# Performance work log

Hardware: AMD Instinct MI355X
Metric: run time of the kernel (lower is better)

The kernel has to match this reference:

```python
import jax, jax.numpy as jnp
import numpy as np

N = 400000      # total atoms
MAXD = 4        # max degree
NDEG = MAXD + 1 # degrees 0..4 (DeepChem min_degree=0)
F0 = 75         # ConvMolFeaturizer atom feature size
B = 16384       # number of graphs (batch_size)
NT = 12         # n_tasks
DIMS = [F0, 15, 20, 27, 36]


def setup_inputs() -> dict:
    key = jax.random.key(0)
    ks = jax.random.split(key, 40)
    inp = {}
    inp["atom_features"] = jax.random.normal(ks[0], (N, F0), jnp.float32)
    i = 1
    for l in range(4):
        fi, fo = DIMS[l], DIMS[l + 1]
        inp[f"Ws{l+1}"] = jax.random.normal(ks[i], (NDEG, fi, fo), jnp.float32) * 0.1; i += 1
        inp[f"Wn{l+1}"] = jax.random.normal(ks[i], (NDEG, fi, fo), jnp.float32) * 0.1; i += 1
        inp[f"b{l+1}"] = jax.random.normal(ks[i], (NDEG, fo), jnp.float32) * 0.1; i += 1
    inp["Wd2"] = jax.random.normal(ks[i], (2 * DIMS[-1], NT * 2), jnp.float32) * 0.1; i += 1
    inp["bd2"] = jnp.zeros((NT * 2,), jnp.float32)
    inp["Wl1"] = jax.random.normal(ks[i], (2 * NT, 96), jnp.float32) * 0.1; i += 1
    inp["bl1"] = jnp.zeros((96,), jnp.float32)
    inp["g1"] = jnp.ones((96,), jnp.float32)
    inp["be1"] = jnp.zeros((96,), jnp.float32)
    inp["Wl2"] = jax.random.normal(ks[i], (96, 63), jnp.float32) * 0.1; i += 1
    inp["bl2"] = jnp.zeros((63,), jnp.float32)
    inp["g2"] = jnp.ones((63,), jnp.float32)
    inp["be2"] = jnp.zeros((63,), jnp.float32)
    inp["Wl3"] = jax.random.normal(ks[i], (63, 138), jnp.float32) * 0.1; i += 1
    inp["bl3"] = jnp.zeros((138,), jnp.float32)
    inp["neighbor_list"] = jax.random.randint(ks[i], (N, MAXD), 0, N, dtype=jnp.int32); i += 1
    inp["degree"] = jax.random.randint(ks[i], (N,), 0, NDEG, dtype=jnp.int32); i += 1
    inp["membership"] = jnp.sort(jax.random.randint(ks[i], (N,), 0, B, dtype=jnp.int32)); i += 1
    inp["batch_size"] = B
    return inp


def _graph_conv(x, Ws, Wn, b, nbr, deg_onehot, nmask):
    # gather neighbor features and sum over (masked) neighbor slots: [N, Fin]
    nsum = (x[nbr] * nmask).sum(axis=1)
    # per-degree affine (DeepChem: separate self/neighbor weights per degree)
    pre = (jnp.einsum('nf,dfg->ndg', x, Ws)
           + jnp.einsum('nf,dfg->ndg', nsum, Wn)
           + b[None])                              # [N, NDEG, Fout]
    out = jnp.einsum('nd,ndg->ng', deg_onehot, pre)  # select row for atom's degree
    return jax.nn.selu(out)


def _bn(x, g, b, eps=1e-5):
    m = x.mean(axis=0)
    v = x.var(axis=0)
    return (x - m) * jax.lax.rsqrt(v + eps) * g + b


def reference(atom_features, Ws1, Wn1, b1, Ws2, Wn2, b2, Ws3, Wn3, b3,
              Ws4, Wn4, b4, Wd2, bd2, Wl1, bl1, g1, be1,
              Wl2, bl2, g2, be2, Wl3, bl3,
              neighbor_list, degree, membership, batch_size):
    deg_onehot = jax.nn.one_hot(degree, NDEG, dtype=atom_features.dtype)
    nmask = (jnp.arange(MAXD, dtype=degree.dtype)[None, :] < degree[:, None])
    nmask = nmask.astype(atom_features.dtype)[:, :, None]          # [N, MAXD, 1]

    x = _graph_conv(atom_features, Ws1, Wn1, b1, neighbor_list, deg_onehot, nmask)
    x = _graph_conv(x, Ws2, Wn2, b2, neighbor_list, deg_onehot, nmask)
    x = _graph_conv(x, Ws3, Wn3, b3, neighbor_list, deg_onehot, nmask)
    x = _graph_conv(x, Ws4, Wn4, b4, neighbor_list, deg_onehot, nmask)

    # GraphGather readout: concat(segment_sum, segment_max) then selu
    s = jax.ops.segment_sum(x, membership, num_segments=batch_size,
                            indices_are_sorted=True)
    m = jax.ops.segment_max(x, membership, num_segments=batch_size,
                            indices_are_sorted=True)
    m = jnp.where(jnp.isfinite(m), m, 0.0)  # empty graphs -> 0
    r = jax.nn.selu(jnp.concatenate([s, m], axis=1))               # [B, 72]

    logits = (r @ Wd2 + bd2).reshape(batch_size, -1, 2)            # [B, NT, 2]
    p = jax.nn.softmax(logits, axis=-1).reshape(batch_size, -1)    # [B, 2*NT]

    h = jax.nn.relu(_bn(p @ Wl1 + bl1, g1, be1))
    h = jax.nn.relu(_bn(h @ Wl2 + bl2, g2, be2))
    return jax.nn.sigmoid(h @ Wl3 + bl3)                            # [B, 138]
```

## Files before the change

kernel.cpp:

```cpp
#include <hip/hip_runtime.h>
#include <hip/hip_bf16.h>

#define N_ATOMS 400000
#define MAX_D   4
#define NDEG_   5
#define B_GR    16384
#define NTASK   12
#define AT      256
#define TA      64
#define NTHR    512
#define PADCAP  401408

typedef float float4u __attribute__((ext_vector_type(4), aligned(4)));

__device__ __forceinline__ float selu_f(float x) {
    const float a = 1.6732632423543772f, s = 1.0507009873554805f;
    return x > 0.f ? s * x : s * a * (__expf(x) - 1.f);
}

__device__ __forceinline__ unsigned short f2bf(float x) {
    unsigned int u = __float_as_uint(x);
    return (unsigned short)((u + 0x7FFFu + ((u >> 16) & 1u)) >> 16);
}
__device__ __forceinline__ float bf2f(unsigned int s) {
    return __uint_as_float(s << 16);
}

__global__ void zero_kernel(int* ctr) {
    if (threadIdx.x < 10) ctr[threadIdx.x] = 0;
}

__launch_bounds__(256)
__global__ void fill_kernel(int* idx, int* degs_s, int4* nbrs_s, int4* nbro_s) {
    const int e = blockIdx.x * 256 + threadIdx.x;
    if (e < PADCAP) {
        idx[e] = -1;
        degs_s[e] = -1;
        nbrs_s[e] = make_int4(0, 0, 0, 0);
        nbro_s[e] = make_int4(0, 0, 0, 0);
    }
}

__launch_bounds__(256)
__global__ void hist_kernel(const int* __restrict__ deg, int* ctr) {
    __shared__ int h[NDEG_];
    if (threadIdx.x < NDEG_) h[threadIdx.x] = 0;
    __syncthreads();
    for (int i = blockIdx.x * 256 + threadIdx.x; i < N_ATOMS; i += gridDim.x * 256)
        atomicAdd(&h[deg[i]], 1);
    __syncthreads();
    if (threadIdx.x < NDEG_ && h[threadIdx.x]) atomicAdd(&ctr[threadIdx.x], h[threadIdx.x]);
}

__global__ void offsets_kernel(int* ctr) {
    if (threadIdx.x == 0) {
        int run = 0;
        for (int d = 0; d < NDEG_; ++d) {
            ctr[10 + d] = run;
            run += ctr[d];
            run = (run + AT - 1) & ~(AT - 1);
        }
        ctr[15] = run;
    }
}

__launch_bounds__(256)
__global__ void scatter_kernel(const int* __restrict__ deg, int* ctr,
                               int* idx, int* rank, int* degs_s) {
    __shared__ int h[NDEG_];
    __shared__ int base[NDEG_];
    const int i = blockIdx.x * 256 + threadIdx.x;
    const int d = (i < N_ATOMS) ? deg[i] : -1;
    if (threadIdx.x < NDEG_) h[threadIdx.x] = 0;
    __syncthreads();
    int intra = 0;
    if (i < N_ATOMS) intra = atomicAdd(&h[d], 1);
    __syncthreads();
    if (threadIdx.x < NDEG_ && h[threadIdx.x] > 0)
        base[threadIdx.x] = atomicAdd(&ctr[5 + threadIdx.x], h[threadIdx.x]);
    __syncthreads();
    if (i < N_ATOMS) {
        const int p = ctr[10 + d] + base[d] + intra;
        idx[p] = i;
        rank[i] = p;
        degs_s[p] = d;
    }
}

__launch_bounds__(256)
__global__ void nbrprep_kernel(const int* __restrict__ nbr, const int* __restrict__ rank,
                               int4* __restrict__ nbrs_s, int4* __restrict__ nbro_s) {
    const int i = blockIdx.x * 256 + threadIdx.x;
    if (i >= N_ATOMS) return;
    const int p = rank[i];
    const int4 nb = *reinterpret_cast<const int4*>(nbr + (size_t)i * MAX_D);
    nbro_s[p] = nb;
    nbrs_s[p] = make_int4(rank[nb.x], rank[nb.y], rank[nb.z], rank[nb.w]);
}

__launch_bounds__(NTHR)
__global__ void conv1_project(const float* __restrict__ af,
                              const float* __restrict__ Ws1,
                              const float* __restrict__ Wn1,
                              const float* __restrict__ b1,
                              const int*   __restrict__ degs_s,
                              const int*   __restrict__ idx,
                              float*       __restrict__ S,
                              unsigned short* __restrict__ Z)
{
    __shared__ float xt[TA][76];
    __shared__ int s_a[TA];

    const int pb = blockIdx.x * TA;
    const int dfirst = degs_s[pb];
    if (dfirst < 0) return;
    const int tid = threadIdx.x;

    if (tid < TA) {
        int a = idx[pb + tid];
        s_a[tid] = (a < 0) ? 0 : a;
    }
    __syncthreads();

    #pragma unroll 2
    for (int e = tid; e < TA * 18; e += NTHR) {
        const int al = e / 18, f4 = e - al * 18;
        *(float4u*)&xt[al][f4 * 4] = *(const float4u*)(af + (size_t)s_a[al] * 75 + f4 * 4);
    }
    for (int e = tid; e < TA * 3; e += NTHR) {
        const int al = e / 3, r = e - al * 3;
        xt[al][72 + r] = af[(size_t)s_a[al] * 75 + 72 + r];
    }
    __syncthreads();

    const int w = __builtin_amdgcn_readfirstlane(tid >> 6);
    const int l = tid & 63;

    if (w < 4) {
        const float* __restrict__ wn = Wn1 + (size_t)(w + 1) * 75 * 15;
        float acc[15];
        #pragma unroll
        for (int o = 0; o < 15; ++o) acc[o] = 0.f;
        for (int f4 = 0; f4 < 18; ++f4) {
            const float4u xv = *(const float4u*)&xt[l][f4 * 4];
            #pragma unroll
            for (int k = 0; k < 4; ++k) {
                const float* __restrict__ wf = wn + (f4 * 4 + k) * 15;
                #pragma unroll
                for (int o = 0; o < 15; ++o) acc[o] = fmaf(xv[k], wf[o], acc[o]);
            }
        }
        #pragma unroll
        for (int k = 0; k < 3; ++k) {
            const float xv = xt[l][72 + k];
            const float* __restrict__ wf = wn + (72 + k) * 15;
            #pragma unroll
            for (int o = 0; o < 15; ++o) acc[o] = fmaf(xv, wf[o], acc[o]);
        }
        unsigned short zr[16];
        #pragma unroll
        for (int o = 0; o < 15; ++o) zr[o] = f2bf(acc[o]);
        zr[15] = 0;
        unsigned short* zp = Z + ((size_t)w * PADCAP + pb + l) * 16;
        ((int4*)zp)[0] = ((const int4*)zr)[0];
        ((int4*)zp)[1] = ((const int4*)zr)[1];
    } else {
        const int o0 = (w - 4) * 4;
        const int d = __builtin_amdgcn_readfirstlane(dfirst);
        const float* __restrict__ wsp = Ws1 + (size_t)d * 75 * 15 + o0;
        const float* __restrict__ bb  = b1 + d * 15 + o0;
        float acc[4];
        #pragma unroll
        for (int oo = 0; oo < 4; ++oo) acc[oo] = (o0 + oo < 15) ? bb[oo] : 0.f;
        for (int f4 = 0; f4 < 18; ++f4) {
            const float4u xv = *(const float4u*)&xt[l][f4 * 4];
            #pragma unroll
            for (int k = 0; k < 4; ++k) {
                const float* __restrict__ wf = wsp + (f4 * 4 + k) * 15;
                #pragma unroll
                for (int oo = 0; oo < 4; ++oo)
                    if (o0 + oo < 15) acc[oo] = fmaf(xv[k], wf[oo], acc[oo]);
            }
        }
        #pragma unroll
        for (int k = 0; k < 3; ++k) {
            const float xv = xt[l][72 + k];
            const float* __restrict__ wf = wsp + (72 + k) * 15;
            #pragma unroll
            for (int oo = 0; oo < 4; ++oo)
                if (o0 + oo < 15) acc[oo] = fmaf(xv, wf[oo], acc[oo]);
        }
        float4u sv = {acc[0], acc[1], acc[2], acc[3]};
        *(float4u*)(S + (size_t)(pb + l) * 16 + o0) = sv;
    }
}

template<int DEG>
__device__ __forceinline__ void combine_body(const float* __restrict__ S,
                                             const unsigned short* __restrict__ Z,
                                             const int4* __restrict__ nbrs_s,
                                             float* __restrict__ x1, int p)
{
    float acc[16];
    #pragma unroll
    for (int q = 0; q < 4; ++q)
        *(float4u*)&acc[q * 4] = *(const float4u*)(S + (size_t)p * 16 + q * 4);

    if (DEG > 0) {
        const int4 nb = nbrs_s[p];
        const int nbid[4] = {nb.x, nb.y, nb.z, nb.w};
        #pragma unroll
        for (int j = 0; j < DEG; ++j) {
            const unsigned short* zp = Z + ((size_t)(DEG - 1) * PADCAP + nbid[j]) * 16;
            unsigned int zz[8];
            *(int4*)&zz[0] = ((const int4*)zp)[0];
            *(int4*)&zz[4] = ((const int4*)zp)[1];
            #pragma unroll
            for (int o = 0; o < 15; ++o)
                acc[o] += bf2f((zz[o >> 1] >> ((o & 1) * 16)) & 0xffffu);
        }
    }
    #pragma unroll
    for (int o = 0; o < 15; ++o)
        x1[(size_t)p * 15 + o] = selu_f(acc[o]);
}

__launch_bounds__(256)
__global__ void conv1_combine(const float* __restrict__ S,
                              const unsigned short* __restrict__ Z,
                              const int4* __restrict__ nbrs_s,
                              const int*  __restrict__ degs_s,
                              float*      __restrict__ x1)
{
    const int base = blockIdx.x * 256;
    const int dfirst = degs_s[base];
    if (dfirst < 0) return;
    const int p = base + threadIdx.x;
    switch (__builtin_amdgcn_readfirstlane(dfirst)) {
    case 0: combine_body<0>(S, Z, nbrs_s, x1, p); break;
    case 1: combine_body<1>(S, Z, nbrs_s, x1, p); break;
    case 2: combine_body<2>(S, Z, nbrs_s, x1, p); break;
    case 3: combine_body<3>(S, Z, nbrs_s, x1, p); break;
    default: combine_body<4>(S, Z, nbrs_s, x1, p); break;
    }
}

template<int FI, int FIP, int FO, bool SCATTER_OUT, int DEG>
__device__ __forceinline__ void conv_body(const float* __restrict__ x,
                                          const float* __restrict__ Ws,
                                          const float* __restrict__ Wn,
                                          const float* __restrict__ bias,
                                          const int*   __restrict__ idx,
                                          float*       __restrict__ outs,
                                          float (*__restrict__ xt)[FIP],
                                          float (*__restrict__ nt)[FIP],
                                          const int*  s_a,
                                          const int4* s_nb,
                                          int pb, int tid)
{
    #pragma unroll 2
    for (int e = tid; e < TA * FI; e += NTHR) {
        const int al = e / FI, f = e - al * FI;
        const int4 nb = s_nb[al];
        const float xv = x[(size_t)s_a[al] * FI + f];
        float s = 0.f;
        if (DEG > 0) s += x[(size_t)nb.x * FI + f];
        if (DEG > 1) s += x[(size_t)nb.y * FI + f];
        if (DEG > 2) s += x[(size_t)nb.z * FI + f];
        if (DEG > 3) s += x[(size_t)nb.w * FI + f];
        xt[al][f] = xv;
        nt[al][f] = s;
    }
    __syncthreads();

    const int w = __builtin_amdgcn_readfirstlane(tid >> 6);
    const int l = tid & 63;
    constexpr int OPG = (FO + 7) / 8;
    const int o0 = w * OPG;
    const float* __restrict__ wsd = Ws + (DEG * FI) * FO + o0;
    const float* __restrict__ wnd = Wn + (DEG * FI) * FO + o0;
    const float* __restrict__ bb  = bias + DEG * FO + o0;

    float acc[OPG];
    #pragma unroll
    for (int oo = 0; oo < OPG; ++oo)
        acc[oo] = (o0 + oo < FO) ? bb[oo] : 0.f;

    for (int f = 0; f < FI; ++f) {
        const float xv = xt[l][f];
        const float nv = nt[l][f];
        const float* __restrict__ wsf = wsd + f * FO;
        const float* __restrict__ wnf = wnd + f * FO;
        #pragma unroll
        for (int oo = 0; oo < OPG; ++oo) {
            if (o0 + oo < FO)
                acc[oo] = fmaf(xv, wsf[oo], fmaf(nv, wnf[oo], acc[oo]));
        }
    }

    int row; bool store;
    if (SCATTER_OUT) { row = idx[pb + l]; store = (row >= 0); }
    else             { row = pb + l;      store = true; }
    if (store) {
        float* __restrict__ orow = outs + (size_t)row * FO + o0;
        #pragma unroll
        for (int oo = 0; oo < OPG; ++oo)
            if (o0 + oo < FO) orow[oo] = selu_f(acc[oo]);
    }
}

template<int FI, int FIP, int FO, bool SCATTER_OUT>
__launch_bounds__(NTHR)
__global__ void conv_fused5(const float* __restrict__ x,
                            const int4*  __restrict__ nbr_,
                            const float* __restrict__ Ws,
                            const float* __restrict__ Wn,
                            const float* __restrict__ bias,
                            const int*   __restrict__ degs_s,
                            const int*   __restrict__ idx,
                            float*       __restrict__ outs)
{
    __shared__ float xt[TA][FIP];
    __shared__ float nt[TA][FIP];
    __shared__ int   s_a[TA];
    __shared__ int4  s_nb[TA];

    const int pb = blockIdx.x * TA;
    const int dfirst = degs_s[pb];
    if (dfirst < 0) return;
    const int tid = threadIdx.x;

    if (tid < TA) {
        const int p = pb + tid;
        s_a[tid] = p;
        s_nb[tid] = nbr_[p];
    }
    __syncthreads();

    switch (__builtin_amdgcn_readfirstlane(dfirst)) {
    case 0: conv_body<FI, FIP, FO, SCATTER_OUT, 0>(x, Ws, Wn, bias, idx, outs, xt, nt, s_a, s_nb, pb, tid); break;
    case 1: conv_body<FI, FIP, FO, SCATTER_OUT, 1>(x, Ws, Wn, bias, idx, outs, xt, nt, s_a, s_nb, pb, tid); break;
    case 2: conv_body<FI, FIP, FO, SCATTER_OUT, 2>(x, Ws, Wn, bias, idx, outs, xt, nt, s_a, s_nb, pb, tid); break;
    case 3: conv_body<FI, FIP, FO, SCATTER_OUT, 3>(x, Ws, Wn, bias, idx, outs, xt, nt, s_a, s_nb, pb, tid); break;
    default: conv_body<FI, FIP, FO, SCATTER_OUT, 4>(x, Ws, Wn, bias, idx, outs, xt, nt, s_a, s_nb, pb, tid); break;
    }
}

__launch_bounds__(64)
__global__ void readout_kernel(const float* __restrict__ x4o,
                               const int*   __restrict__ mem,
                               const float* __restrict__ Wd2,
                               const float* __restrict__ bd2,
                               float*       __restrict__ p)
{
    const int g = blockIdx.x;
    const int t = threadIdx.x;

    int lo = 0, hi = N_ATOMS;
    while (lo < hi) { int mid = (lo + hi) >> 1; if (mem[mid] < g) lo = mid + 1; else hi = mid; }
    int lo2 = lo, hi2 = N_ATOMS;
    while (lo2 < hi2) { int mid = (lo2 + hi2) >> 1; if (mem[mid] < g + 1) lo2 = mid + 1; else hi2 = mid; }

    __shared__ float r[72];
    if (t < 36) {
        float s = 0.f, m = -3.4e38f;
        for (int a = lo; a < lo2; ++a) {
            float v = x4o[(size_t)a * 36 + t];
            s += v;
            m = fmaxf(m, v);
        }
        if (lo2 == lo) m = 0.f;
        r[t]      = selu_f(s);
        r[36 + t] = selu_f(m);
    }
    __syncthreads();
    if (t < 24) {
        float acc = bd2[t];
        #pragma unroll
        for (int f = 0; f < 72; ++f) acc += r[f] * Wd2[f * 24 + t];
        float part = __shfl_xor(acc, 1);
        p[g * 24 + t] = 1.f / (1.f + __expf(part - acc));
    }
}

__launch_bounds__(256)
__global__ void dense1_kernel(const float* __restrict__ p,
                              const float* __restrict__ Wl1,
                              const float* __restrict__ bl1,
                              float*       __restrict__ y1)
{
    const int idx = blockIdx.x * 256 + threadIdx.x;
    if (idx >= B_GR * 96) return;
    const int row = idx / 96, c = idx - row * 96;
    float acc = bl1[c];
    const float* pr = p + row * 24;
    #pragma unroll
    for (int f = 0; f < 24; ++f) acc += pr[f] * Wl1[f * 96 + c];
    y1[idx] = acc;
}

template<int C>
__launch_bounds__(256)
__global__ void stats_kernel(const float* __restrict__ y, float* __restrict__ st)
{
    const int c = blockIdx.x;
    float s = 0.f, q = 0.f;
    for (int r = threadIdx.x; r < B_GR; r += 256) {
        const float v = y[r * C + c];
        s += v; q += v * v;
    }
    __shared__ float ss[256], qq[256];
    ss[threadIdx.x] = s; qq[threadIdx.x] = q;
    __syncthreads();
    for (int off = 128; off > 0; off >>= 1) {
        if (threadIdx.x < off) {
            ss[threadIdx.x] += ss[threadIdx.x + off];
            qq[threadIdx.x] += qq[threadIdx.x + off];
        }
        __syncthreads();
    }
    if (threadIdx.x == 0) {
        const float mean = ss[0] / (float)B_GR;
        const float var  = qq[0] / (float)B_GR - mean * mean;
        st[c]     = mean;
        st[C + c] = rsqrtf(var + 1e-5f);
    }
}

__launch_bounds__(256)
__global__ void dense2_kernel(const float* __restrict__ y1,
                              const float* __restrict__ st1,
                              const float* __restrict__ g1,
                              const float* __restrict__ be1,
                              const float* __restrict__ Wl2,
                              const float* __restrict__ bl2,
                              float*       __restrict__ y2)
{
    __shared__ float h[4 * 96];
    const int r0 = blockIdx.x * 4;
    for (int e = threadIdx.x; e < 4 * 96; e += 256) {
        const int rr = e / 96, c = e - rr * 96;
        float v = y1[(r0 + rr) * 96 + c];
        v = (v - st1[c]) * st1[96 + c] * g1[c] + be1[c];
        h[e] = fmaxf(v, 0.f);
    }
    __syncthreads();
    for (int e = threadIdx.x; e < 4 * 63; e += 256) {
        const int rr = e / 63, o = e - rr * 63;
        float acc = bl2[o];
        #pragma unroll
        for (int f = 0; f < 96; ++f) acc += h[rr * 96 + f] * Wl2[f * 63 + o];
        y2[(r0 + rr) * 63 + o] = acc;
    }
}

__launch_bounds__(320)
__global__ void dense3_kernel(const float* __restrict__ y2,
                              const float* __restrict__ st2,
                              const float* __restrict__ g2,
                              const float* __restrict__ be2,
                              const float* __restrict__ Wl3,
                              const float* __restrict__ bl3,
                              float*       __restrict__ out)
{
    __shared__ float h[2 * 63];
    const int r0 = blockIdx.x * 2;
    for (int e = threadIdx.x; e < 2 * 63; e += 320) {
        const int rr = e / 63, c = e - rr * 63;
        float v = y2[(r0 + rr) * 63 + c];
        v = (v - st2[c]) * st2[63 + c] * g2[c] + be2[c];
        h[e] = fmaxf(v, 0.f);
    }
    __syncthreads();
    for (int e = threadIdx.x; e < 2 * 138; e += 320) {
        const int rr = e / 138, o = e - rr * 138;
        float acc = bl3[o];
        #pragma unroll
        for (int f = 0; f < 63; ++f) acc += h[rr * 63 + f] * Wl3[f * 138 + o];
        out[(r0 + rr) * 138 + o] = 1.f / (1.f + __expf(-acc));
    }
}

extern "C" void kernel_launch(void* const* d_in, const int* in_sizes, int n_in,
                              void* d_out, int out_size, void* d_ws, size_t ws_size,
                              hipStream_t stream)
{
    (void)in_sizes; (void)n_in; (void)out_size; (void)ws_size;

    const float* af  = (const float*)d_in[0];
    const float* Ws1 = (const float*)d_in[1];
    const float* Wn1 = (const float*)d_in[2];
    const float* b1  = (const float*)d_in[3];
    const float* Ws2 = (const float*)d_in[4];
    const float* Wn2 = (const float*)d_in[5];
    const float* b2  = (const float*)d_in[6];
    const float* Ws3 = (const float*)d_in[7];
    const float* Wn3 = (const float*)d_in[8];
    const float* b3  = (const float*)d_in[9];
    const float* Ws4 = (const float*)d_in[10];
    const float* Wn4 = (const float*)d_in[11];
    const float* b4  = (const float*)d_in[12];
    const float* Wd2 = (const float*)d_in[13];
    const float* bd2 = (const float*)d_in[14];
    const float* Wl1 = (const float*)d_in[15];
    const float* bl1 = (const float*)d_in[16];
    const float* g1  = (const float*)d_in[17];
    const float* be1 = (const float*)d_in[18];
    const float* Wl2 = (const float*)d_in[19];
    const float* bl2 = (const float*)d_in[20];
    const float* g2  = (const float*)d_in[21];
    const float* be2 = (const float*)d_in[22];
    const float* Wl3 = (const float*)d_in[23];
    const float* bl3 = (const float*)d_in[24];
    const int*   nbr = (const int*)d_in[25];
    const int*   deg = (const int*)d_in[26];
    const int*   mem = (const int*)d_in[27];

    float* ws = (float*)d_ws;
    float* A = ws;
    float* B = A + (size_t)PADCAP * 27;
    float* Zr = B + (size_t)PADCAP * 36;
    int*   idx    = (int*)(Zr + (size_t)PADCAP * 32);
    int*   rank   = idx + PADCAP;
    int*   degs_s = rank + N_ATOMS;
    int4*  nbrs_s = (int4*)(degs_s + PADCAP);
    int4*  nbro_s = nbrs_s + PADCAP;
    int*   ctr    = (int*)(nbro_s + PADCAP);

    float* x1  = A;
    float* Sb  = B;
    unsigned short* Zb = (unsigned short*)Zr;
    float* x2  = B;
    float* x3  = A;
    float* x4o = B;
    float* p   = A;
    float* y1  = A + 393216;
    float* y2  = A + 393216 + 1572864;
    float* st1 = A + 393216 + 1572864 + 1032192;
    float* st2 = st1 + 192;

    zero_kernel<<<1, 16, 0, stream>>>(ctr);
    fill_kernel<<<PADCAP / 256, 256, 0, stream>>>(idx, degs_s, nbrs_s, nbro_s);
    hist_kernel<<<1024, 256, 0, stream>>>(deg, ctr);
    offsets_kernel<<<1, 1, 0, stream>>>(ctr);
    scatter_kernel<<<(N_ATOMS + 255) / 256, 256, 0, stream>>>(deg, ctr, idx, rank, degs_s);
    nbrprep_kernel<<<(N_ATOMS + 255) / 256, 256, 0, stream>>>(nbr, rank, nbrs_s, nbro_s);

    conv1_project<<<PADCAP / TA, NTHR, 0, stream>>>(af, Ws1, Wn1, b1, degs_s, idx, Sb, Zb);
    conv1_combine<<<PADCAP / 256, 256, 0, stream>>>(Sb, Zb, nbrs_s, degs_s, x1);

    conv_fused5<15, 17, 20, false><<<PADCAP / TA, NTHR, 0, stream>>>
        (x1, nbrs_s, Ws2, Wn2, b2, degs_s, idx, x2);
    conv_fused5<20, 21, 27, false><<<PADCAP / TA, NTHR, 0, stream>>>
        (x2, nbrs_s, Ws3, Wn3, b3, degs_s, idx, x3);
    conv_fused5<27, 29, 36, true ><<<PADCAP / TA, NTHR, 0, stream>>>
        (x3, nbrs_s, Ws4, Wn4, b4, degs_s, idx, x4o);

    readout_kernel<<<B_GR, 64, 0, stream>>>(x4o, mem, Wd2, bd2, p);

    dense1_kernel<<<(B_GR * 96) / 256, 256, 0, stream>>>(p, Wl1, bl1, y1);
    stats_kernel<96><<<96, 256, 0, stream>>>(y1, st1);
    dense2_kernel<<<B_GR / 4, 256, 0, stream>>>(y1, st1, g1, be1, Wl2, bl2, y2);
    stats_kernel<63><<<63, 256, 0, stream>>>(y2, st2);
    dense3_kernel<<<B_GR / 2, 320, 0, stream>>>(y2, st2, g2, be2, Wl3, bl3, (float*)d_out);
}
```

Baseline: 710.8 us.

## Merge conv1 projection waves and split combine across four threads per atom

The layer-1 projection kernel drops from 8 to 4 waves per block. Each wave now computes both its neighbor-weight Z projection and a 4-column slice of the self projection, so each LDS row of features is read once for both. The combine kernel assigns four threads per atom, each handling a 4-output slice with 8-byte gathers, which raises parallelism and shortens per-thread work. Per-thread register pressure in projection goes up and block count per atom tile is unchanged, so occupancy and latency hiding shift.

```diff
diff --git a/kernel.cpp b/kernel.cpp
--- a/kernel.cpp
+++ b/kernel.cpp
@@ -98,7 +98,7 @@
     nbrs_s[p] = make_int4(rank[nb.x], rank[nb.y], rank[nb.z], rank[nb.w]);
 }
 
-__launch_bounds__(NTHR)
+__launch_bounds__(256)
 __global__ void conv1_project(const float* __restrict__ af,
                               const float* __restrict__ Ws1,
                               const float* __restrict__ Wn1,
@@ -123,11 +123,11 @@
     __syncthreads();
 
     #pragma unroll 2
-    for (int e = tid; e < TA * 18; e += NTHR) {
+    for (int e = tid; e < TA * 18; e += 256) {
         const int al = e / 18, f4 = e - al * 18;
         *(float4u*)&xt[al][f4 * 4] = *(const float4u*)(af + (size_t)s_a[al] * 75 + f4 * 4);
     }
-    for (int e = tid; e < TA * 3; e += NTHR) {
+    for (int e = tid; e < TA * 3; e += 256) {
         const int al = e / 3, r = e - al * 3;
         xt[al][72 + r] = af[(size_t)s_a[al] * 75 + 72 + r];
     }
@@ -135,94 +135,90 @@
 
     const int w = __builtin_amdgcn_readfirstlane(tid >> 6);
     const int l = tid & 63;
-
-    if (w < 4) {
-        const float* __restrict__ wn = Wn1 + (size_t)(w + 1) * 75 * 15;
-        float acc[15];
-        #pragma unroll
-        for (int o = 0; o < 15; ++o) acc[o] = 0.f;
-        for (int f4 = 0; f4 < 18; ++f4) {
-            const float4u xv = *(const float4u*)&xt[l][f4 * 4];
+    const int d = __builtin_amdgcn_readfirstlane(dfirst);
+    const int o0 = w * 4;
+    const float* __restrict__ wn  = Wn1 + (size_t)(w + 1) * 75 * 15;
+    const float* __restrict__ wsp = Ws1 + (size_t)d * 75 * 15 + o0;
+    const float* __restrict__ bb  = b1 + d * 15 + o0;
+
+    float accz[15];
+    #pragma unroll
+    for (int o = 0; o < 15; ++o) accz[o] = 0.f;
+    float accs[4];
+    #pragma unroll
+    for (int oo = 0; oo < 4; ++oo) accs[oo] = (o0 + oo < 15) ? bb[oo] : 0.f;
+
+    #pragma unroll
+    for (int g = 0; g < 6; ++g) {
+        const float4u c0 = *(const float4u*)&xt[l][(g * 3 + 0) * 4];
+        const float4u c1 = *(const float4u*)&xt[l][(g * 3 + 1) * 4];
+        const float4u c2 = *(const float4u*)&xt[l][(g * 3 + 2) * 4];
+        #pragma unroll
+        for (int c = 0; c < 3; ++c) {
+            const float4u xv = (c == 0) ? c0 : (c == 1) ? c1 : c2;
             #pragma unroll
             for (int k = 0; k < 4; ++k) {
-                const float* __restrict__ wf = wn + (f4 * 4 + k) * 15;
+                const int f = (g * 3 + c) * 4 + k;
+                const float* __restrict__ wfz = wn + f * 15;
+                const float* __restrict__ wfs = wsp + f * 15;
                 #pragma unroll
-                for (int o = 0; o < 15; ++o) acc[o] = fmaf(xv[k], wf[o], acc[o]);
+                for (int o = 0; o < 15; ++o) accz[o] = fmaf(xv[k], wfz[o], accz[o]);
+                #pragma unroll
+                for (int oo = 0; oo < 4; ++oo)
+                    if (o0 + oo < 15) accs[oo] = fmaf(xv[k], wfs[oo], accs[oo]);
             }
         }
-        #pragma unroll
-        for (int k = 0; k < 3; ++k) {
-            const float xv = xt[l][72 + k];
-            const float* __restrict__ wf = wn + (72 + k) * 15;
-            #pragma unroll
-            for (int o = 0; o < 15; ++o) acc[o] = fmaf(xv, wf[o], acc[o]);
-        }
-        unsigned short zr[16];
-        #pragma unroll
-        for (int o = 0; o < 15; ++o) zr[o] = f2bf(acc[o]);
-        zr[15] = 0;
-        unsigned short* zp = Z + ((size_t)w * PADCAP + pb + l) * 16;
-        ((int4*)zp)[0] = ((const int4*)zr)[0];
-        ((int4*)zp)[1] = ((const int4*)zr)[1];
-    } else {
-        const int o0 = (w - 4) * 4;
-        const int d = __builtin_amdgcn_readfirstlane(dfirst);
-        const float* __restrict__ wsp = Ws1 + (size_t)d * 75 * 15 + o0;
-        const float* __restrict__ bb  = b1 + d * 15 + o0;
-        float acc[4];
-        #pragma unroll
-        for (int oo = 0; oo < 4; ++oo) acc[oo] = (o0 + oo < 15) ? bb[oo] : 0.f;
-        for (int f4 = 0; f4 < 18; ++f4) {
-            const float4u xv = *(const float4u*)&xt[l][f4 * 4];
-            #pragma unroll
-            for (int k = 0; k < 4; ++k) {
-                const float* __restrict__ wf = wsp + (f4 * 4 + k) * 15;
-                #pragma unroll
-                for (int oo = 0; oo < 4; ++oo)
-                    if (o0 + oo < 15) acc[oo] = fmaf(xv[k], wf[oo], acc[oo]);
-            }
-        }
-        #pragma unroll
-        for (int k = 0; k < 3; ++k) {
-            const float xv = xt[l][72 + k];
-            const float* __restrict__ wf = wsp + (72 + k) * 15;
-            #pragma unroll
-            for (int oo = 0; oo < 4; ++oo)
-                if (o0 + oo < 15) acc[oo] = fmaf(xv, wf[oo], acc[oo]);
-        }
-        float4u sv = {acc[0], acc[1], acc[2], acc[3]};
-        *(float4u*)(S + (size_t)(pb + l) * 16 + o0) = sv;
-    }
+    }
+    #pragma unroll
+    for (int k = 0; k < 3; ++k) {
+        const float xv = xt[l][72 + k];
+        const float* __restrict__ wfz = wn + (72 + k) * 15;
+        const float* __restrict__ wfs = wsp + (72 + k) * 15;
+        #pragma unroll
+        for (int o = 0; o < 15; ++o) accz[o] = fmaf(xv, wfz[o], accz[o]);
+        #pragma unroll
+        for (int oo = 0; oo < 4; ++oo)
+            if (o0 + oo < 15) accs[oo] = fmaf(xv, wfs[oo], accs[oo]);
+    }
+
+    unsigned short zr[16];
+    #pragma unroll
+    for (int o = 0; o < 15; ++o) zr[o] = f2bf(accz[o]);
+    zr[15] = 0;
+    unsigned short* zp = Z + ((size_t)w * PADCAP + pb + l) * 16;
+    ((int4*)zp)[0] = ((const int4*)zr)[0];
+    ((int4*)zp)[1] = ((const int4*)zr)[1];
+
+    float4u sv = {accs[0], accs[1], accs[2], accs[3]};
+    *(float4u*)(S + (size_t)(pb + l) * 16 + o0) = sv;
 }
 
 template<int DEG>
 __device__ __forceinline__ void combine_body(const float* __restrict__ S,
                                              const unsigned short* __restrict__ Z,
                                              const int4* __restrict__ nbrs_s,
-                                             float* __restrict__ x1, int p)
-{
-    float acc[16];
-    #pragma unroll
-    for (int q = 0; q < 4; ++q)
-        *(float4u*)&acc[q * 4] = *(const float4u*)(S + (size_t)p * 16 + q * 4);
+                                             float* __restrict__ x1, int p, int q)
+{
+    const int o0 = q * 4;
+    float4u acc = *(const float4u*)(S + (size_t)p * 16 + o0);
 
     if (DEG > 0) {
         const int4 nb = nbrs_s[p];
         const int nbid[4] = {nb.x, nb.y, nb.z, nb.w};
         #pragma unroll
         for (int j = 0; j < DEG; ++j) {
-            const unsigned short* zp = Z + ((size_t)(DEG - 1) * PADCAP + nbid[j]) * 16;
-            unsigned int zz[8];
-            *(int4*)&zz[0] = ((const int4*)zp)[0];
-            *(int4*)&zz[4] = ((const int4*)zp)[1];
-            #pragma unroll
-            for (int o = 0; o < 15; ++o)
-                acc[o] += bf2f((zz[o >> 1] >> ((o & 1) * 16)) & 0xffffu);
+            const unsigned short* zp =
+                Z + ((size_t)(DEG - 1) * PADCAP + nbid[j]) * 16 + o0;
+            const uint2 zz = *(const uint2*)zp;
+            acc[0] += bf2f(zz.x & 0xffffu);
+            acc[1] += bf2f(zz.x >> 16);
+            acc[2] += bf2f(zz.y & 0xffffu);
+            acc[3] += bf2f(zz.y >> 16);
         }
     }
     #pragma unroll
-    for (int o = 0; o < 15; ++o)
-        x1[(size_t)p * 15 + o] = selu_f(acc[o]);
+    for (int k = 0; k < 4; ++k)
+        if (o0 + k < 15) x1[(size_t)p * 15 + o0 + k] = selu_f(acc[k]);
 }
 
 __launch_bounds__(256)
@@ -232,16 +228,17 @@
                               const int*  __restrict__ degs_s,
                               float*      __restrict__ x1)
 {
-    const int base = blockIdx.x * 256;
+    const int base = blockIdx.x * 64;
     const int dfirst = degs_s[base];
     if (dfirst < 0) return;
-    const int p = base + threadIdx.x;
+    const int p = base + (threadIdx.x >> 2);
+    const int q = threadIdx.x & 3;
     switch (__builtin_amdgcn_readfirstlane(dfirst)) {
-    case 0: combine_body<0>(S, Z, nbrs_s, x1, p); break;
-    case 1: combine_body<1>(S, Z, nbrs_s, x1, p); break;
-    case 2: combine_body<2>(S, Z, nbrs_s, x1, p); break;
-    case 3: combine_body<3>(S, Z, nbrs_s, x1, p); break;
-    default: combine_body<4>(S, Z, nbrs_s, x1, p); break;
+    case 0: combine_body<0>(S, Z, nbrs_s, x1, p, q); break;
+    case 1: combine_body<1>(S, Z, nbrs_s, x1, p, q); break;
+    case 2: combine_body<2>(S, Z, nbrs_s, x1, p, q); break;
+    case 3: combine_body<3>(S, Z, nbrs_s, x1, p, q); break;
+    default: combine_body<4>(S, Z, nbrs_s, x1, p, q); break;
     }
 }
 
@@ -546,8 +543,8 @@
     scatter_kernel<<<(N_ATOMS + 255) / 256, 256, 0, stream>>>(deg, ctr, idx, rank, degs_s);
     nbrprep_kernel<<<(N_ATOMS + 255) / 256, 256, 0, stream>>>(nbr, rank, nbrs_s, nbro_s);
 
-    conv1_project<<<PADCAP / TA, NTHR, 0, stream>>>(af, Ws1, Wn1, b1, degs_s, idx, Sb, Zb);
-    conv1_combine<<<PADCAP / 256, 256, 0, stream>>>(Sb, Zb, nbrs_s, degs_s, x1);
+    conv1_project<<<PADCAP / TA, 256, 0, stream>>>(af, Ws1, Wn1, b1, degs_s, idx, Sb, Zb);
+    conv1_combine<<<PADCAP / 64, 256, 0, stream>>>(Sb, Zb, nbrs_s, degs_s, x1);
 
     conv_fused5<15, 17, 20, false><<<PADCAP / TA, NTHR, 0, stream>>>
         (x1, nbrs_s, Ws2, Wn2, b2, degs_s, idx, x2);
```

Result: slower. 877.3 us (+23.4%).
